# Kernel optimization log

Hardware: AMD Instinct MI355X
Metric: run time of the kernel (lower is better)

## Reference

```python
import jax, jax.numpy as jnp
import numpy as np
import math

B, N, D_MODEL, D_QK, D_V = 8, 2048, 512, 64, 64
NEG_INF = float('-inf')

def setup_inputs() -> dict:
    key = jax.random.key(0)
    k1, k2, k3, k4, k5 = jax.random.split(key, 5)
    mask = jax.random.randint(k1, (B, N, N), 0, 2).astype(bool)
    x_key_value = jax.random.normal(k2, (B, N, D_MODEL), dtype=jnp.float32)
    wk = jax.random.normal(k3, (D_MODEL, D_QK), dtype=jnp.float32) * 0.02
    wq = jax.random.normal(k4, (D_MODEL, D_QK), dtype=jnp.float32) * 0.02
    wv = jax.random.normal(k5, (D_MODEL, D_V), dtype=jnp.float32) * 0.02
    return {"mask": mask, "x_key_value": x_key_value, "wk": wk, "wq": wq, "wv": wv}

def reference(mask, x_key_value, wk, wq, wv):
    # self-attention: x_query defaults to x_key_value
    div = math.sqrt(wk.shape[1])
    k = x_key_value @ wk          # [n, j, d_qk]
    q = x_key_value @ wq          # [n, i, d_qk]
    v = x_key_value @ wv          # [n, j, d_v]
    mat = jnp.einsum('nik,njk->nij', q, k) / div
    mat = jnp.where(mask, mat, NEG_INF)
    portion = jax.nn.softmax(mat, axis=2)
    return jnp.einsum('nij,njk->nik', portion, v)
```

## Files before the change

### kernel.cpp

```cpp
#include <hip/hip_runtime.h>
#include <hip/hip_bf16.h>

typedef __attribute__((ext_vector_type(8))) short bf16x8;
typedef __attribute__((ext_vector_type(4))) float f32x4;
typedef __hip_bfloat16 bf16;
typedef unsigned long long ull;

#define BATCH 8
#define SEQ   2048
#define DMODEL 512
#define DHEAD 64
#define ROWS (BATCH * SEQ)
#define SCALE_LOG2 0.1803368801f

static __device__ inline short f2bf(float f) {
    union { __hip_bfloat16 h; short s; } u;
    u.h = __float2bfloat16(f);
    return u.s;
}

__global__ __launch_bounds__(256) void pack_mask_kernel(
    const int* __restrict__ mask, ull* __restrict__ pm)
{
    const int wgl = (blockIdx.x * 256 + threadIdx.x) >> 6;
    const int lane = threadIdx.x & 63;
    const uint4* src = (const uint4*)mask;
    const size_t cbase = (size_t)wgl * 16;

    for (int it = 0; it < 4; ++it) {
        size_t c0 = cbase + it * 4;
        uint4 v0 = src[(c0 + 0) * 64 + lane];
        uint4 v1 = src[(c0 + 1) * 64 + lane];
        uint4 v2 = src[(c0 + 2) * 64 + lane];
        uint4 v3 = src[(c0 + 3) * 64 + lane];
        ull b00 = __ballot(v0.x != 0), b01 = __ballot(v0.y != 0);
        ull b02 = __ballot(v0.z != 0), b03 = __ballot(v0.w != 0);
        ull b10 = __ballot(v1.x != 0), b11 = __ballot(v1.y != 0);
        ull b12 = __ballot(v1.z != 0), b13 = __ballot(v1.w != 0);
        ull b20 = __ballot(v2.x != 0), b21 = __ballot(v2.y != 0);
        ull b22 = __ballot(v2.z != 0), b23 = __ballot(v2.w != 0);
        ull b30 = __ballot(v3.x != 0), b31 = __ballot(v3.y != 0);
        ull b32 = __ballot(v3.z != 0), b33 = __ballot(v3.w != 0);
        if (lane == 0) {
            ull* d = pm + c0 * 4;
            d[0] = b00; d[1] = b01; d[2]  = b02; d[3]  = b03;
            d[4] = b10; d[5] = b11; d[6]  = b12; d[7]  = b13;
            d[8] = b20; d[9] = b21; d[10] = b22; d[11] = b23;
            d[12] = b30; d[13] = b31; d[14] = b32; d[15] = b33;
        }
    }
}

__global__ __launch_bounds__(256) void transpose_w_kernel(
    const float* __restrict__ wq, const float* __restrict__ wk,
    const float* __restrict__ wv, bf16* __restrict__ wt)
{
    const int s  = blockIdx.x / 8;
    const int kt = blockIdx.x % 8;
    const float* w = (s == 0) ? wq : ((s == 1) ? wk : wv);

    __shared__ float Ts[64][68];

    const int tid = threadIdx.x;
    int nr = tid >> 4;
    int n4 = (tid & 15) * 4;
#pragma unroll
    for (int p = 0; p < 4; ++p) {
        int k = 16 * p + nr;
        float4 v = *(const float4*)(w + (size_t)(kt * 64 + k) * DHEAD + n4);
        Ts[k][n4] = v.x; Ts[k][n4 + 1] = v.y; Ts[k][n4 + 2] = v.z; Ts[k][n4 + 3] = v.w;
    }
    __syncthreads();
#pragma unroll
    for (int p = 0; p < 2; ++p) {
        int cc = tid + p * 256;
        int n = cc >> 3;
        int kk = (cc & 7) * 8;
        bf16x8 o;
#pragma unroll
        for (int e = 0; e < 8; ++e) o[e] = f2bf(Ts[kk + e][n]);
        *(bf16x8*)(wt + (size_t)(s * 64 + n) * DMODEL + kt * 64 + kk) = o;
    }
}

__global__ __launch_bounds__(256) void proj_kernel(
    const float* __restrict__ x, const bf16* __restrict__ wt,
    bf16* __restrict__ Q, bf16* __restrict__ K, bf16* __restrict__ Vt)
{
    const int bb = blockIdx.x & 7;
    const int tt = blockIdx.x >> 3;
    const int r0 = bb * SEQ + tt * 16;
    const int tid = threadIdx.x;
    const int lane = tid & 63;
    const int cq = tid >> 6;
    const int l15 = lane & 15;
    const int quad = lane >> 4;

    __shared__ __align__(8) bf16 Vs[64][20];

    f32x4 acc[3] = {};

    const float* xp = x + (size_t)(r0 + l15) * DMODEL + quad * 8;

#pragma unroll
    for (int k0 = 0; k0 < DMODEL; k0 += 64) {
        float4 xa = *(const float4*)(xp + k0);
        float4 xb = *(const float4*)(xp + k0 + 4);
        float4 xc = *(const float4*)(xp + k0 + 32);
        float4 xd = *(const float4*)(xp + k0 + 36);
        bf16x8 a0, a1;
        a0[0] = f2bf(xa.x); a0[1] = f2bf(xa.y); a0[2] = f2bf(xa.z); a0[3] = f2bf(xa.w);
        a0[4] = f2bf(xb.x); a0[5] = f2bf(xb.y); a0[6] = f2bf(xb.z); a0[7] = f2bf(xb.w);
        a1[0] = f2bf(xc.x); a1[1] = f2bf(xc.y); a1[2] = f2bf(xc.z); a1[3] = f2bf(xc.w);
        a1[4] = f2bf(xd.x); a1[5] = f2bf(xd.y); a1[6] = f2bf(xd.z); a1[7] = f2bf(xd.w);

#pragma unroll
        for (int g = 0; g < 3; ++g) {
            int n = 16 * (3 * cq + g) + l15;
            const bf16* wp = wt + (size_t)n * DMODEL + k0 + quad * 8;
            bf16x8 b0 = *(const bf16x8*)(wp);
            bf16x8 b1 = *(const bf16x8*)(wp + 32);
            acc[g] = __builtin_amdgcn_mfma_f32_16x16x32_bf16(a0, b0, acc[g], 0, 0, 0);
            acc[g] = __builtin_amdgcn_mfma_f32_16x16x32_bf16(a1, b1, acc[g], 0, 0, 0);
        }
    }

#pragma unroll
    for (int g = 0; g < 3; ++g) {
        int ng = 16 * (3 * cq + g) + l15;
        int sel = ng >> 6;
        int col = ng & 63;
#pragma unroll
        for (int r = 0; r < 4; ++r) {
            int rowl = quad * 4 + r;
            int row = r0 + rowl;
            union { __hip_bfloat16 h; bf16 b; } u;
            u.h = __float2bfloat16(acc[g][r]);
            if (sel == 0)      Q[(size_t)row * DHEAD + col] = u.b;
            else if (sel == 1) K[(size_t)row * DHEAD + col] = u.b;
            else               Vs[col][rowl] = u.b;
        }
    }
    __syncthreads();

    {
        int d = tid >> 2;
        int j4 = (tid & 3) * 4;
        uint2 payload = *(const uint2*)(&Vs[d][j4]);
        *(uint2*)(Vt + ((size_t)(bb * DHEAD + d)) * SEQ + tt * 16 + j4) = payload;
    }
}

__global__ __launch_bounds__(256) void flash_kernel(
    const bf16* __restrict__ Q, const bf16* __restrict__ K,
    const bf16* __restrict__ Vt, const ull* __restrict__ pm,
    float* __restrict__ out)
{
    const int b = blockIdx.x;
    const int q0 = blockIdx.y * 16;
    const int tid = threadIdx.x;
    const int lane = tid & 63;
    const int wid = tid >> 6;
    const int l15 = lane & 15;
    const int quad = lane >> 4;

    __shared__ __align__(16) bf16 Ps[4][16][72];
    __shared__ float Om[4][16][64];
    __shared__ float Lw[4][16];

    const int sh = l15 >> 2;
    const ull* p0 = pm + ((size_t)(b * SEQ + q0 + quad * 4 + 0) * 8 + wid * 2) * 4 + (l15 & 3);
    const ull* p1 = pm + ((size_t)(b * SEQ + q0 + quad * 4 + 1) * 8 + wid * 2) * 4 + (l15 & 3);
    const ull* p2 = pm + ((size_t)(b * SEQ + q0 + quad * 4 + 2) * 8 + wid * 2) * 4 + (l15 & 3);
    const ull* p3 = pm + ((size_t)(b * SEQ + q0 + quad * 4 + 3) * 8 + wid * 2) * 4 + (l15 & 3);

    const bf16* qp = Q + ((size_t)(b * SEQ + q0 + l15)) * DHEAD + quad * 8;
    bf16x8 aQ0 = *(const bf16x8*)(qp);
    bf16x8 aQ1 = *(const bf16x8*)(qp + 32);

    f32x4 oacc[4] = {};
    float lsum[4] = {0.f, 0.f, 0.f, 0.f};

    const int jbase = wid * (SEQ / 4);

#pragma unroll
    for (int jt = 0; jt < 8; ++jt) {
        const int ch = jt >> 2;
        const int s = jt & 3;
        const int j0 = jbase + jt * 64;

        ull w0 = p0[ch * 4] >> sh;
        ull w1 = p1[ch * 4] >> sh;
        ull w2 = p2[ch * 4] >> sh;
        ull w3 = p3[ch * 4] >> sh;

        f32x4 sacc[4] = {};
#pragma unroll
        for (int c = 0; c < 4; ++c) {
            const bf16* kp = K + ((size_t)(b * SEQ + j0 + 16 * c + l15)) * DHEAD + quad * 8;
            bf16x8 b0 = *(const bf16x8*)(kp);
            bf16x8 b1 = *(const bf16x8*)(kp + 32);
            sacc[c] = __builtin_amdgcn_mfma_f32_16x16x32_bf16(aQ0, b0, sacc[c], 0, 0, 0);
            sacc[c] = __builtin_amdgcn_mfma_f32_16x16x32_bf16(aQ1, b1, sacc[c], 0, 0, 0);
        }

#pragma unroll
        for (int c = 0; c < 4; ++c) {
            {
                float e = exp2f(sacc[c][0] * SCALE_LOG2);
                float p = ((w0 >> (16 * s + 4 * c)) & 1ull) ? e : 0.0f;
                lsum[0] += p;
                union { __hip_bfloat16 h; bf16 b; } u; u.h = __float2bfloat16(p);
                Ps[wid][quad * 4 + 0][16 * c + l15] = u.b;
            }
            {
                float e = exp2f(sacc[c][1] * SCALE_LOG2);
                float p = ((w1 >> (16 * s + 4 * c)) & 1ull) ? e : 0.0f;
                lsum[1] += p;
                union { __hip_bfloat16 h; bf16 b; } u; u.h = __float2bfloat16(p);
                Ps[wid][quad * 4 + 1][16 * c + l15] = u.b;
            }
            {
                float e = exp2f(sacc[c][2] * SCALE_LOG2);
                float p = ((w2 >> (16 * s + 4 * c)) & 1ull) ? e : 0.0f;
                lsum[2] += p;
                union { __hip_bfloat16 h; bf16 b; } u; u.h = __float2bfloat16(p);
                Ps[wid][quad * 4 + 2][16 * c + l15] = u.b;
            }
            {
                float e = exp2f(sacc[c][3] * SCALE_LOG2);
                float p = ((w3 >> (16 * s + 4 * c)) & 1ull) ? e : 0.0f;
                lsum[3] += p;
                union { __hip_bfloat16 h; bf16 b; } u; u.h = __float2bfloat16(p);
                Ps[wid][quad * 4 + 3][16 * c + l15] = u.b;
            }
        }

        bf16x8 aP0 = *(const bf16x8*)(&Ps[wid][l15][quad * 8]);
        bf16x8 aP1 = *(const bf16x8*)(&Ps[wid][l15][32 + quad * 8]);
#pragma unroll
        for (int c = 0; c < 4; ++c) {
            const bf16* vp = Vt + ((size_t)b * DHEAD + 16 * c + l15) * SEQ + j0 + quad * 8;
            bf16x8 v0 = *(const bf16x8*)(vp);
            bf16x8 v1 = *(const bf16x8*)(vp + 32);
            oacc[c] = __builtin_amdgcn_mfma_f32_16x16x32_bf16(aP0, v0, oacc[c], 0, 0, 0);
            oacc[c] = __builtin_amdgcn_mfma_f32_16x16x32_bf16(aP1, v1, oacc[c], 0, 0, 0);
        }
    }

#pragma unroll
    for (int r = 0; r < 4; ++r) {
        lsum[r] += __shfl_xor(lsum[r], 1);
        lsum[r] += __shfl_xor(lsum[r], 2);
        lsum[r] += __shfl_xor(lsum[r], 4);
        lsum[r] += __shfl_xor(lsum[r], 8);
    }

#pragma unroll
    for (int c = 0; c < 4; ++c)
#pragma unroll
        for (int r = 0; r < 4; ++r)
            Om[wid][quad * 4 + r][16 * c + l15] = oacc[c][r];
    if (l15 == 0) {
#pragma unroll
        for (int r = 0; r < 4; ++r) Lw[wid][quad * 4 + r] = lsum[r];
    }
    __syncthreads();

    {
        int row = tid >> 4;
        int c0 = (tid & 15) * 4;
        float L = Lw[0][row] + Lw[1][row] + Lw[2][row] + Lw[3][row];
        float invL = 1.0f / L;
        float4 o;
        float* op = (float*)&o;
#pragma unroll
        for (int e = 0; e < 4; ++e) {
            op[e] = (Om[0][row][c0 + e] + Om[1][row][c0 + e] +
                     Om[2][row][c0 + e] + Om[3][row][c0 + e]) * invL;
        }
        *(float4*)(out + ((size_t)(b * SEQ + q0 + row)) * DHEAD + c0) = o;
    }
}

extern "C" void kernel_launch(void* const* d_in, const int* in_sizes, int n_in,
                              void* d_out, int out_size, void* d_ws, size_t ws_size,
                              hipStream_t stream)
{
    const int*   mask = (const int*)d_in[0];
    const float* x    = (const float*)d_in[1];
    const float* wk   = (const float*)d_in[2];
    const float* wq   = (const float*)d_in[3];
    const float* wv   = (const float*)d_in[4];
    float* out = (float*)d_out;

    bf16* Qb = (bf16*)d_ws;
    bf16* Kb = Qb + (size_t)ROWS * DHEAD;
    bf16* Vt = Kb + (size_t)ROWS * DHEAD;
    bf16* Wt = Vt + (size_t)BATCH * DHEAD * SEQ;
    ull*  pm = (ull*)(Wt + 3 * 64 * DMODEL);

    pack_mask_kernel<<<dim3(2048), 256, 0, stream>>>(mask, pm);
    transpose_w_kernel<<<dim3(24), 256, 0, stream>>>(wq, wk, wv, Wt);
    proj_kernel<<<dim3(1024), 256, 0, stream>>>(x, Wt, Qb, Kb, Vt);
    flash_kernel<<<dim3(BATCH, SEQ / 16), 256, 0, stream>>>(Qb, Kb, Vt, pm, out);
}
```

Before: 313.3 us.

## Fuse mask packing into projection kernel and split flash keys over eight waves

Mask bit-packing is merged into the projection launch as a second block role, interleaved with the projection blocks, so the two independent prep stages share one grid and one fewer kernel is launched. The flash kernel now uses 512 threads (8 waves), each covering 256 keys, so every wave loads its mask words once up front. The P staging buffer and the partial-output buffer share one shared-memory region, separated by an added barrier. The cost is a larger cross-wave reduction over 8 partials and a heavier final combine per row.

```diff
diff --git a/kernel.cpp b/kernel.cpp
--- a/kernel.cpp
+++ b/kernel.cpp
@@ -17,38 +17,6 @@
     union { __hip_bfloat16 h; short s; } u;
     u.h = __float2bfloat16(f);
     return u.s;
-}
-
-__global__ __launch_bounds__(256) void pack_mask_kernel(
-    const int* __restrict__ mask, ull* __restrict__ pm)
-{
-    const int wgl = (blockIdx.x * 256 + threadIdx.x) >> 6;
-    const int lane = threadIdx.x & 63;
-    const uint4* src = (const uint4*)mask;
-    const size_t cbase = (size_t)wgl * 16;
-
-    for (int it = 0; it < 4; ++it) {
-        size_t c0 = cbase + it * 4;
-        uint4 v0 = src[(c0 + 0) * 64 + lane];
-        uint4 v1 = src[(c0 + 1) * 64 + lane];
-        uint4 v2 = src[(c0 + 2) * 64 + lane];
-        uint4 v3 = src[(c0 + 3) * 64 + lane];
-        ull b00 = __ballot(v0.x != 0), b01 = __ballot(v0.y != 0);
-        ull b02 = __ballot(v0.z != 0), b03 = __ballot(v0.w != 0);
-        ull b10 = __ballot(v1.x != 0), b11 = __ballot(v1.y != 0);
-        ull b12 = __ballot(v1.z != 0), b13 = __ballot(v1.w != 0);
-        ull b20 = __ballot(v2.x != 0), b21 = __ballot(v2.y != 0);
-        ull b22 = __ballot(v2.z != 0), b23 = __ballot(v2.w != 0);
-        ull b30 = __ballot(v3.x != 0), b31 = __ballot(v3.y != 0);
-        ull b32 = __ballot(v3.z != 0), b33 = __ballot(v3.w != 0);
-        if (lane == 0) {
-            ull* d = pm + c0 * 4;
-            d[0] = b00; d[1] = b01; d[2]  = b02; d[3]  = b03;
-            d[4] = b10; d[5] = b11; d[6]  = b12; d[7]  = b13;
-            d[8] = b20; d[9] = b21; d[10] = b22; d[11] = b23;
-            d[12] = b30; d[13] = b31; d[14] = b32; d[15] = b33;
-        }
-    }
 }
 
 __global__ __launch_bounds__(256) void transpose_w_kernel(
@@ -83,20 +51,57 @@
     }
 }
 
-__global__ __launch_bounds__(256) void proj_kernel(
+__global__ __launch_bounds__(256) void prep_kernel(
     const float* __restrict__ x, const bf16* __restrict__ wt,
-    bf16* __restrict__ Q, bf16* __restrict__ K, bf16* __restrict__ Vt)
+    const int* __restrict__ mask,
+    bf16* __restrict__ Q, bf16* __restrict__ K, bf16* __restrict__ Vt,
+    ull* __restrict__ pm)
 {
-    const int bb = blockIdx.x & 7;
-    const int tt = blockIdx.x >> 3;
+    const int bid = blockIdx.x;
+    const int role = (bid >> 3) & 1;
+    const int sub = ((bid >> 4) << 3) | (bid & 7);
+    const int tid = threadIdx.x;
+
+    __shared__ __align__(8) bf16 Vs[64][20];
+
+    if (role == 1) {
+        const int wgl = sub * 4 + (tid >> 6);
+        const int lane = tid & 63;
+        const uint4* src = (const uint4*)mask;
+        const size_t cbase = (size_t)wgl * 32;
+
+        for (int it = 0; it < 8; ++it) {
+            size_t c0 = cbase + it * 4;
+            uint4 v0 = src[(c0 + 0) * 64 + lane];
+            uint4 v1 = src[(c0 + 1) * 64 + lane];
+            uint4 v2 = src[(c0 + 2) * 64 + lane];
+            uint4 v3 = src[(c0 + 3) * 64 + lane];
+            ull b00 = __ballot(v0.x != 0), b01 = __ballot(v0.y != 0);
+            ull b02 = __ballot(v0.z != 0), b03 = __ballot(v0.w != 0);
+            ull b10 = __ballot(v1.x != 0), b11 = __ballot(v1.y != 0);
+            ull b12 = __ballot(v1.z != 0), b13 = __ballot(v1.w != 0);
+            ull b20 = __ballot(v2.x != 0), b21 = __ballot(v2.y != 0);
+            ull b22 = __ballot(v2.z != 0), b23 = __ballot(v2.w != 0);
+            ull b30 = __ballot(v3.x != 0), b31 = __ballot(v3.y != 0);
+            ull b32 = __ballot(v3.z != 0), b33 = __ballot(v3.w != 0);
+            if (lane == 0) {
+                ull* d = pm + c0 * 4;
+                d[0]  = b00; d[1]  = b01; d[2]  = b02; d[3]  = b03;
+                d[4]  = b10; d[5]  = b11; d[6]  = b12; d[7]  = b13;
+                d[8]  = b20; d[9]  = b21; d[10] = b22; d[11] = b23;
+                d[12] = b30; d[13] = b31; d[14] = b32; d[15] = b33;
+            }
+        }
+        return;
+    }
+
+    const int bb = sub & 7;
+    const int tt = sub >> 3;
     const int r0 = bb * SEQ + tt * 16;
-    const int tid = threadIdx.x;
     const int lane = tid & 63;
     const int cq = tid >> 6;
     const int l15 = lane & 15;
     const int quad = lane >> 4;
-
-    __shared__ __align__(8) bf16 Vs[64][20];
 
     f32x4 acc[3] = {};
 
@@ -151,7 +156,7 @@
     }
 }
 
-__global__ __launch_bounds__(256) void flash_kernel(
+__global__ __launch_bounds__(512, 8) void flash_kernel(
     const bf16* __restrict__ Q, const bf16* __restrict__ K,
     const bf16* __restrict__ Vt, const ull* __restrict__ pm,
     float* __restrict__ out)
@@ -164,15 +169,17 @@
     const int l15 = lane & 15;
     const int quad = lane >> 4;
 
-    __shared__ __align__(16) bf16 Ps[4][16][72];
-    __shared__ float Om[4][16][64];
-    __shared__ float Lw[4][16];
+    __shared__ __align__(16) unsigned char smem[8 * 16 * 64 * 4];
+    bf16  (*Ps)[16][72] = (bf16 (*)[16][72])smem;
+    float (*Om)[16][64] = (float(*)[16][64])smem;
+    __shared__ float Lw[8][16];
 
     const int sh = l15 >> 2;
-    const ull* p0 = pm + ((size_t)(b * SEQ + q0 + quad * 4 + 0) * 8 + wid * 2) * 4 + (l15 & 3);
-    const ull* p1 = pm + ((size_t)(b * SEQ + q0 + quad * 4 + 1) * 8 + wid * 2) * 4 + (l15 & 3);
-    const ull* p2 = pm + ((size_t)(b * SEQ + q0 + quad * 4 + 2) * 8 + wid * 2) * 4 + (l15 & 3);
-    const ull* p3 = pm + ((size_t)(b * SEQ + q0 + quad * 4 + 3) * 8 + wid * 2) * 4 + (l15 & 3);
+    const size_t rb = (size_t)(b * SEQ + q0 + quad * 4);
+    ull w0 = pm[((rb + 0) * 8 + wid) * 4 + (l15 & 3)] >> sh;
+    ull w1 = pm[((rb + 1) * 8 + wid) * 4 + (l15 & 3)] >> sh;
+    ull w2 = pm[((rb + 2) * 8 + wid) * 4 + (l15 & 3)] >> sh;
+    ull w3 = pm[((rb + 3) * 8 + wid) * 4 + (l15 & 3)] >> sh;
 
     const bf16* qp = Q + ((size_t)(b * SEQ + q0 + l15)) * DHEAD + quad * 8;
     bf16x8 aQ0 = *(const bf16x8*)(qp);
@@ -181,18 +188,11 @@
     f32x4 oacc[4] = {};
     float lsum[4] = {0.f, 0.f, 0.f, 0.f};
 
-    const int jbase = wid * (SEQ / 4);
-
-#pragma unroll
-    for (int jt = 0; jt < 8; ++jt) {
-        const int ch = jt >> 2;
-        const int s = jt & 3;
+    const int jbase = wid * 256;
+
+#pragma unroll
+    for (int jt = 0; jt < 4; ++jt) {
         const int j0 = jbase + jt * 64;
-
-        ull w0 = p0[ch * 4] >> sh;
-        ull w1 = p1[ch * 4] >> sh;
-        ull w2 = p2[ch * 4] >> sh;
-        ull w3 = p3[ch * 4] >> sh;
 
         f32x4 sacc[4] = {};
 #pragma unroll
@@ -206,30 +206,31 @@
 
 #pragma unroll
         for (int c = 0; c < 4; ++c) {
+            const int bit = 16 * jt + 4 * c;
             {
                 float e = exp2f(sacc[c][0] * SCALE_LOG2);
-                float p = ((w0 >> (16 * s + 4 * c)) & 1ull) ? e : 0.0f;
+                float p = ((w0 >> bit) & 1ull) ? e : 0.0f;
                 lsum[0] += p;
                 union { __hip_bfloat16 h; bf16 b; } u; u.h = __float2bfloat16(p);
                 Ps[wid][quad * 4 + 0][16 * c + l15] = u.b;
             }
             {
                 float e = exp2f(sacc[c][1] * SCALE_LOG2);
-                float p = ((w1 >> (16 * s + 4 * c)) & 1ull) ? e : 0.0f;
+                float p = ((w1 >> bit) & 1ull) ? e : 0.0f;
                 lsum[1] += p;
                 union { __hip_bfloat16 h; bf16 b; } u; u.h = __float2bfloat16(p);
                 Ps[wid][quad * 4 + 1][16 * c + l15] = u.b;
             }
             {
                 float e = exp2f(sacc[c][2] * SCALE_LOG2);
-                float p = ((w2 >> (16 * s + 4 * c)) & 1ull) ? e : 0.0f;
+                float p = ((w2 >> bit) & 1ull) ? e : 0.0f;
                 lsum[2] += p;
                 union { __hip_bfloat16 h; bf16 b; } u; u.h = __float2bfloat16(p);
                 Ps[wid][quad * 4 + 2][16 * c + l15] = u.b;
             }
             {
                 float e = exp2f(sacc[c][3] * SCALE_LOG2);
-                float p = ((w3 >> (16 * s + 4 * c)) & 1ull) ? e : 0.0f;
+                float p = ((w3 >> bit) & 1ull) ? e : 0.0f;
                 lsum[3] += p;
                 union { __hip_bfloat16 h; bf16 b; } u; u.h = __float2bfloat16(p);
                 Ps[wid][quad * 4 + 3][16 * c + l15] = u.b;
@@ -248,6 +249,8 @@
         }
     }
 
+    __syncthreads();
+
 #pragma unroll
     for (int r = 0; r < 4; ++r) {
         lsum[r] += __shfl_xor(lsum[r], 1);
@@ -268,18 +271,21 @@
     __syncthreads();
 
     {
-        int row = tid >> 4;
-        int c0 = (tid & 15) * 4;
-        float L = Lw[0][row] + Lw[1][row] + Lw[2][row] + Lw[3][row];
+        int row = tid >> 5;
+        int c0 = (tid & 31) * 2;
+        float L = Lw[0][row] + Lw[1][row] + Lw[2][row] + Lw[3][row] +
+                  Lw[4][row] + Lw[5][row] + Lw[6][row] + Lw[7][row];
         float invL = 1.0f / L;
-        float4 o;
+        float2 o;
         float* op = (float*)&o;
 #pragma unroll
-        for (int e = 0; e < 4; ++e) {
-            op[e] = (Om[0][row][c0 + e] + Om[1][row][c0 + e] +
-                     Om[2][row][c0 + e] + Om[3][row][c0 + e]) * invL;
-        }
-        *(float4*)(out + ((size_t)(b * SEQ + q0 + row)) * DHEAD + c0) = o;
+        for (int e = 0; e < 2; ++e) {
+            float s = 0.f;
+#pragma unroll
+            for (int k = 0; k < 8; ++k) s += Om[k][row][c0 + e];
+            op[e] = s * invL;
+        }
+        *(float2*)(out + ((size_t)(b * SEQ + q0 + row)) * DHEAD + c0) = o;
     }
 }
 
@@ -300,8 +306,7 @@
     bf16* Wt = Vt + (size_t)BATCH * DHEAD * SEQ;
     ull*  pm = (ull*)(Wt + 3 * 64 * DMODEL);
 
-    pack_mask_kernel<<<dim3(2048), 256, 0, stream>>>(mask, pm);
     transpose_w_kernel<<<dim3(24), 256, 0, stream>>>(wq, wk, wv, Wt);
-    proj_kernel<<<dim3(1024), 256, 0, stream>>>(x, Wt, Qb, Kb, Vt);
-    flash_kernel<<<dim3(BATCH, SEQ / 16), 256, 0, stream>>>(Qb, Kb, Vt, pm, out);
-}
+    prep_kernel<<<dim3(2048), 256, 0, stream>>>(x, Wt, mask, Qb, Kb, Vt, pm);
+    flash_kernel<<<dim3(BATCH, SEQ / 16), 512, 0, stream>>>(Qb, Kb, Vt, pm, out);
+}
```

New measurement: 360.8 us. 1.15x slower.
